# Kernel tuning notes

Measured on AMD Instinct MI355X. Metric: run time of the kernel, lower is better.

## Reference

```python
import jax, jax.numpy as jnp
import numpy as np
from jax import lax

K = 8          # neighbors
LOSS_NORM = 2  # Lp norm over coords


def setup_inputs() -> dict:
    key = jax.random.key(0)
    k1, k2, k3 = jax.random.split(key, 3)
    B, N = 4, 8192
    return {
        "pc_source": jax.random.normal(k1, (B, N, 3), dtype=jnp.float32),
        "pc_target": jax.random.normal(k2, (B, N, 3), dtype=jnp.float32),
        "pred_flow": jax.random.normal(k3, (B, N, 3), dtype=jnp.float32),
    }


def _knn_idx(query, points, k):
    # query: [B,N,3], points: [B,M,3] -> idx [B,N,k] of k nearest points per query
    # squared euclidean pairwise distances (ranking-equivalent to euclidean)
    q2 = jnp.sum(query * query, axis=-1, keepdims=True)          # [B,N,1]
    p2 = jnp.sum(points * points, axis=-1)[:, None, :]           # [B,1,M]
    d2 = q2 + p2 - 2.0 * jnp.einsum("bnd,bmd->bnm", query, points)  # [B,N,M]
    _, idx = lax.top_k(-d2, k)                                   # smallest-k
    return idx


def _gather_points(points, idx):
    # points: [B,M,3], idx: [B,N,k] -> [B,N,k,3]
    return jax.vmap(lambda p, i: p[i])(points, idx)


def reference(pc_source, pc_target, pred_flow):
    pc_pred = pc_source + pred_flow                               # [B,N,3]

    # knn indices are detached in the original (idx.detach())
    idx1 = _knn_idx(lax.stop_gradient(pc_pred), lax.stop_gradient(pc_target), K)
    nn1 = _gather_points(pc_target, idx1)                         # [B,N,K,3]
    diff1 = pc_pred[:, :, None, :] - nn1                          # [B,N,K,3]
    dist1 = jnp.linalg.norm(diff1, ord=LOSS_NORM, axis=-1).mean(axis=-1)  # [B,N]

    idx2 = _knn_idx(lax.stop_gradient(pc_target), lax.stop_gradient(pc_pred), K)
    nn2 = _gather_points(pc_pred, idx2)                           # [B,M,K,3]
    diff2 = pc_target[:, :, None, :] - nn2
    dist2 = jnp.linalg.norm(diff2, ord=LOSS_NORM, axis=-1).mean(axis=-1)  # [B,M]

    return (dist1 + dist2).mean()
```

## Files before the change

### kernel.cpp

```cpp
#include <hip/hip_runtime.h>
#include <math.h>

constexpr int B = 4;
constexpr int N = 8192;
constexpr int KNN = 8;
constexpr int NCELL = 4096;
constexpr int GSIZE = 16;
constexpr int NGRP = N / GSIZE;
constexpr int QPB = 64;
constexpr int WAVES = 8;
constexpr int NCB = 2 * B;

__device__ __forceinline__ void insert8(float (&d)[KNN], float tv) {
  float n0 = fminf(d[0], tv);
  float n1 = __builtin_amdgcn_fmed3f(d[0], d[1], tv);
  float n2 = __builtin_amdgcn_fmed3f(d[1], d[2], tv);
  float n3 = __builtin_amdgcn_fmed3f(d[2], d[3], tv);
  float n4 = __builtin_amdgcn_fmed3f(d[3], d[4], tv);
  float n5 = __builtin_amdgcn_fmed3f(d[4], d[5], tv);
  float n6 = __builtin_amdgcn_fmed3f(d[5], d[6], tv);
  float n7 = __builtin_amdgcn_fmed3f(d[6], d[7], tv);
  d[0] = n0; d[1] = n1; d[2] = n2; d[3] = n3;
  d[4] = n4; d[5] = n5; d[6] = n6; d[7] = n7;
}

__device__ __forceinline__ int morton3(int x, int y, int z) {
  int m = 0;
#pragma unroll
  for (int b = 0; b < 4; ++b)
    m |= (((x >> b) & 1) << (3 * b + 2)) | (((y >> b) & 1) << (3 * b + 1)) |
         (((z >> b) & 1) << (3 * b + 0));
  return m;
}

__device__ __forceinline__ int point_cell(float x, float y, float z) {
  int cx = (int)fminf(fmaxf((x + 4.0f) * 2.0f, 0.0f), 15.0f);
  int cy = (int)fminf(fmaxf((y + 4.0f) * 2.0f, 0.0f), 15.0f);
  int cz = (int)fminf(fmaxf((z + 4.0f) * 2.0f, 0.0f), 15.0f);
  return morton3(cx, cy, cz);
}

__global__ __launch_bounds__(1024) void prep_kernel(
    const float* __restrict__ src, const float* __restrict__ tgt,
    const float* __restrict__ flow, float4* __restrict__ pred_s,
    float4* __restrict__ tgt_s, float4* __restrict__ gbox,
    float* __restrict__ out) {
  __shared__ int hist[NCELL];
  __shared__ int wsum[16];
  __shared__ float4 pts[N];
  int tid = threadIdx.x, cb = blockIdx.x;
  int cloud = cb >> 2, batch = cb & 3;
  if (cb == 0 && tid == 0) out[0] = 0.0f;

  for (int i = tid; i < NCELL; i += 1024) hist[i] = 0;
  __syncthreads();

  const float* __restrict__ bp = (cloud == 0 ? src : tgt) + batch * N * 3;
  const float* __restrict__ bf = flow + batch * N * 3;
  float4 pt[8];
  int cell[8];
#pragma unroll
  for (int k = 0; k < 8; ++k) {
    int i = k * 1024 + tid;
    float x = bp[3 * i + 0], y = bp[3 * i + 1], z = bp[3 * i + 2];
    if (cloud == 0) { x += bf[3 * i + 0]; y += bf[3 * i + 1]; z += bf[3 * i + 2]; }
    pt[k] = make_float4(x, y, z, 0.5f * (x * x + y * y + z * z));
    cell[k] = point_cell(x, y, z);
    atomicAdd(&hist[cell[k]], 1);
  }
  __syncthreads();

  int b4 = tid * 4;
  int h0v = hist[b4 + 0], h1v = hist[b4 + 1];
  int h2v = hist[b4 + 2], h3v = hist[b4 + 3];
  int s = h0v + h1v + h2v + h3v;
  int lane = tid & 63, w = tid >> 6;
  int incl = s;
#pragma unroll
  for (int off = 1; off < 64; off <<= 1) {
    int u = __shfl_up(incl, off, 64);
    if (lane >= off) incl += u;
  }
  if (lane == 63) wsum[w] = incl;
  __syncthreads();
  if (tid < 16) {
    int v = wsum[tid], inc = v;
#pragma unroll
    for (int off = 1; off < 16; off <<= 1) {
      int u = __shfl_up(inc, off, 64);
      if (tid >= off) inc += u;
    }
    wsum[tid] = inc - v;
  }
  __syncthreads();
  int run = incl - s + wsum[w];
  hist[b4 + 0] = run; run += h0v;
  hist[b4 + 1] = run; run += h1v;
  hist[b4 + 2] = run; run += h2v;
  hist[b4 + 3] = run;
  __syncthreads();

#pragma unroll
  for (int k = 0; k < 8; ++k) {
    int pos = atomicAdd(&hist[cell[k]], 1);
    pts[pos] = pt[k];
  }
  __syncthreads();

  float4* __restrict__ dst = (cloud == 0 ? pred_s : tgt_s) + batch * N;
#pragma unroll
  for (int k = 0; k < 8; ++k) dst[k * 1024 + tid] = pts[k * 1024 + tid];

  if (tid < NGRP) {
    float lx = INFINITY, ly = INFINITY, lz = INFINITY;
    float hx = -INFINITY, hy = -INFINITY, hz = -INFINITY;
#pragma unroll
    for (int t = 0; t < GSIZE; ++t) {
      int j = (t + tid) & 15;
      float4 p = pts[tid * GSIZE + j];
      lx = fminf(lx, p.x); ly = fminf(ly, p.y); lz = fminf(lz, p.z);
      hx = fmaxf(hx, p.x); hy = fmaxf(hy, p.y); hz = fmaxf(hz, p.z);
    }
    gbox[cb * 2 * NGRP + 2 * tid + 0] = make_float4(lx, ly, lz, 0.0f);
    gbox[cb * 2 * NGRP + 2 * tid + 1] = make_float4(hx, hy, hz, 0.0f);
  }
}

__global__ __launch_bounds__(512, 8) void chamfer_kernel(
    const float4* __restrict__ pred_s, const float4* __restrict__ tgt_s,
    const float4* __restrict__ aabb, float* __restrict__ out) {
  int blk = blockIdx.x;
  int dir = blk >> 9;
  int batch = (blk >> 7) & 3;
  int chunk = blk & 127;
  const float4* __restrict__ qarr = (dir == 0 ? pred_s : tgt_s) + batch * N;
  const float4* __restrict__ parr = (dir == 0 ? tgt_s : pred_s) + batch * N;
  int ccb = (dir == 0 ? 4 + batch : batch);
  const float4* __restrict__ gb = aabb + ccb * (2 * NGRP);

  int lane = threadIdx.x & 63;
  int wv = __builtin_amdgcn_readfirstlane(threadIdx.x >> 6);

  __shared__ float4 boxes[2 * NGRP];
  __shared__ float part[WAVES][QPB][KNN + 1];

  for (int i = threadIdx.x; i < 2 * NGRP; i += 512) boxes[i] = gb[i];

  float4 q = qarr[chunk * QPB + lane];
  float nqx = -q.x, nqy = -q.y, nqz = -q.z;
  float two_qw = 2.0f * q.w;

  float d[KNN];
#pragma unroll
  for (int i = 0; i < KNN; ++i) d[i] = INFINITY;
  float thr = INFINITY;

  __syncthreads();

  int tc = (chunk * 4 + 6 - wv) >> 3;
  tc = max(0, min(63, tc));

  auto step = [&](int t) {
    int g = t * 8 + wv;
    float4 lo = boxes[2 * g + 0];
    float4 hi = boxes[2 * g + 1];
    float dx = fmaxf(fmaxf(lo.x - q.x, q.x - hi.x), 0.0f);
    float dy = fmaxf(fmaxf(lo.y - q.y, q.y - hi.y), 0.0f);
    float dz = fmaxf(fmaxf(lo.z - q.z, q.z - hi.z), 0.0f);
    float md = __builtin_fmaf(dx, dx, __builtin_fmaf(dy, dy, dz * dz));
    if (__ballot(md < thr)) {
      const float4* __restrict__ gp = parr + g * GSIZE;
#pragma unroll
      for (int j = 0; j < GSIZE; ++j) {
        float4 p = gp[j];
        float tv = __builtin_fmaf(nqx, p.x, __builtin_fmaf(nqy, p.y,
                   __builtin_fmaf(nqz, p.z, p.w)));
        insert8(d, tv);
      }
      float cand = __builtin_fmaf(2.0f, d[KNN - 1], two_qw) * 1.00001f + 1e-6f;
      thr = fminf(thr, cand);
    }
  };

  step(tc);
  if (tc + 1 < 64) step(tc + 1);

  part[wv][lane][0] = thr;
  __syncthreads();
  float tmin = part[0][lane][0];
#pragma unroll
  for (int s = 1; s < WAVES; ++s) tmin = fminf(tmin, part[s][lane][0]);
  thr = fminf(thr, tmin);
  __syncthreads();

  for (int t = tc + 2; t < 64; ++t) step(t);
  for (int t = tc - 1; t >= 0; --t) step(t);

#pragma unroll
  for (int i = 0; i < KNN; ++i) part[wv][lane][i] = d[i];
  __syncthreads();

  if (wv == 0) {
    float m[KNN];
#pragma unroll
    for (int i = 0; i < KNN; ++i) m[i] = part[0][lane][i];
    for (int s = 1; s < WAVES; ++s) {
#pragma unroll
      for (int i = 0; i < KNN; ++i) insert8(m, part[s][lane][i]);
    }
    float s_ = 0.0f;
#pragma unroll
    for (int i = 0; i < KNN; ++i) {
      float d2 = fmaxf(__builtin_fmaf(2.0f, m[i], two_qw), 0.0f);
      s_ += sqrtf(d2);
    }
    float val = s_ * (1.0f / KNN);
    for (int off = 32; off; off >>= 1) val += __shfl_down(val, off, 64);
    if (lane == 0) atomicAdd(out, val * (1.0f / (B * N)));
  }
}

extern "C" void kernel_launch(void* const* d_in, const int* in_sizes, int n_in,
                              void* d_out, int out_size, void* d_ws, size_t ws_size,
                              hipStream_t stream) {
  const float* src = (const float*)d_in[0];
  const float* tgt = (const float*)d_in[1];
  const float* flow = (const float*)d_in[2];
  float* out = (float*)d_out;

  float4* pred_s = (float4*)d_ws;
  float4* tgt_s = pred_s + B * N;
  float4* gbox = tgt_s + B * N;

  prep_kernel<<<NCB, 1024, 0, stream>>>(src, tgt, flow, pred_s, tgt_s, gbox,
                                        out);
  chamfer_kernel<<<2 * B * (N / QPB), 512, 0, stream>>>(pred_s, tgt_s, gbox, out);
}
```

Measured before the change: 126.2 us.

## Add window-level bounding boxes for hierarchical pruning and vectorize prep loads

After: 148.5 us. +17.6%, slower.

```diff
diff --git a/kernel.cpp b/kernel.cpp
--- a/kernel.cpp
+++ b/kernel.cpp
@@ -7,6 +7,7 @@
 constexpr int NCELL = 4096;
 constexpr int GSIZE = 16;
 constexpr int NGRP = N / GSIZE;
+constexpr int NWIN = 8;
 constexpr int QPB = 64;
 constexpr int WAVES = 8;
 constexpr int NCB = 2 * B;
@@ -44,10 +45,11 @@
     const float* __restrict__ src, const float* __restrict__ tgt,
     const float* __restrict__ flow, float4* __restrict__ pred_s,
     float4* __restrict__ tgt_s, float4* __restrict__ gbox,
-    float* __restrict__ out) {
+    float4* __restrict__ wbox, float* __restrict__ out) {
   __shared__ int hist[NCELL];
   __shared__ int wsum[16];
   __shared__ float4 pts[N];
+  __shared__ float4 wplo[16], wphi[16];
   int tid = threadIdx.x, cb = blockIdx.x;
   int cloud = cb >> 2, batch = cb & 3;
   if (cb == 0 && tid == 0) out[0] = 0.0f;
@@ -56,14 +58,28 @@
   __syncthreads();
 
   const float* __restrict__ bp = (cloud == 0 ? src : tgt) + batch * N * 3;
-  const float* __restrict__ bf = flow + batch * N * 3;
+  const float4* __restrict__ bp4 = reinterpret_cast<const float4*>(bp);
+  float4 s0 = bp4[6 * tid + 0], s1 = bp4[6 * tid + 1], s2 = bp4[6 * tid + 2];
+  float4 s3 = bp4[6 * tid + 3], s4 = bp4[6 * tid + 4], s5 = bp4[6 * tid + 5];
+  if (cloud == 0) {
+    const float4* __restrict__ bf4 =
+        reinterpret_cast<const float4*>(flow + batch * N * 3);
+    float4 f;
+    f = bf4[6 * tid + 0]; s0.x += f.x; s0.y += f.y; s0.z += f.z; s0.w += f.w;
+    f = bf4[6 * tid + 1]; s1.x += f.x; s1.y += f.y; s1.z += f.z; s1.w += f.w;
+    f = bf4[6 * tid + 2]; s2.x += f.x; s2.y += f.y; s2.z += f.z; s2.w += f.w;
+    f = bf4[6 * tid + 3]; s3.x += f.x; s3.y += f.y; s3.z += f.z; s3.w += f.w;
+    f = bf4[6 * tid + 4]; s4.x += f.x; s4.y += f.y; s4.z += f.z; s4.w += f.w;
+    f = bf4[6 * tid + 5]; s5.x += f.x; s5.y += f.y; s5.z += f.z; s5.w += f.w;
+  }
+  float px[8] = {s0.x, s0.w, s1.z, s2.y, s3.x, s3.w, s4.z, s5.y};
+  float py[8] = {s0.y, s1.x, s1.w, s2.z, s3.y, s4.x, s4.w, s5.z};
+  float pz[8] = {s0.z, s1.y, s2.x, s2.w, s3.z, s4.y, s5.x, s5.w};
   float4 pt[8];
   int cell[8];
 #pragma unroll
   for (int k = 0; k < 8; ++k) {
-    int i = k * 1024 + tid;
-    float x = bp[3 * i + 0], y = bp[3 * i + 1], z = bp[3 * i + 2];
-    if (cloud == 0) { x += bf[3 * i + 0]; y += bf[3 * i + 1]; z += bf[3 * i + 2]; }
+    float x = px[k], y = py[k], z = pz[k];
     pt[k] = make_float4(x, y, z, 0.5f * (x * x + y * y + z * z));
     cell[k] = point_cell(x, y, z);
     atomicAdd(&hist[cell[k]], 1);
@@ -111,6 +127,40 @@
 #pragma unroll
   for (int k = 0; k < 8; ++k) dst[k * 1024 + tid] = pts[k * 1024 + tid];
 
+  {
+    float lx = INFINITY, ly = INFINITY, lz = INFINITY;
+    float hx = -INFINITY, hy = -INFINITY, hz = -INFINITY;
+#pragma unroll
+    for (int t = 0; t < 8; ++t) {
+      int j = (t + tid) & 7;
+      float4 p = pts[tid * 8 + j];
+      lx = fminf(lx, p.x); ly = fminf(ly, p.y); lz = fminf(lz, p.z);
+      hx = fmaxf(hx, p.x); hy = fmaxf(hy, p.y); hz = fmaxf(hz, p.z);
+    }
+#pragma unroll
+    for (int m = 1; m < 64; m <<= 1) {
+      lx = fminf(lx, __shfl_xor(lx, m, 64));
+      ly = fminf(ly, __shfl_xor(ly, m, 64));
+      lz = fminf(lz, __shfl_xor(lz, m, 64));
+      hx = fmaxf(hx, __shfl_xor(hx, m, 64));
+      hy = fmaxf(hy, __shfl_xor(hy, m, 64));
+      hz = fmaxf(hz, __shfl_xor(hz, m, 64));
+    }
+    if (lane == 0) {
+      wplo[w] = make_float4(lx, ly, lz, 0.0f);
+      wphi[w] = make_float4(hx, hy, hz, 0.0f);
+    }
+  }
+  __syncthreads();
+  if (tid < NWIN) {
+    float4 a = wplo[2 * tid], b2 = wplo[2 * tid + 1];
+    float4 c = wphi[2 * tid], e = wphi[2 * tid + 1];
+    wbox[cb * 2 * NWIN + 2 * tid + 0] =
+        make_float4(fminf(a.x, b2.x), fminf(a.y, b2.y), fminf(a.z, b2.z), 0.0f);
+    wbox[cb * 2 * NWIN + 2 * tid + 1] =
+        make_float4(fmaxf(c.x, e.x), fmaxf(c.y, e.y), fmaxf(c.z, e.z), 0.0f);
+  }
+
   if (tid < NGRP) {
     float lx = INFINITY, ly = INFINITY, lz = INFINITY;
     float hx = -INFINITY, hy = -INFINITY, hz = -INFINITY;
@@ -128,7 +178,8 @@
 
 __global__ __launch_bounds__(512, 8) void chamfer_kernel(
     const float4* __restrict__ pred_s, const float4* __restrict__ tgt_s,
-    const float4* __restrict__ aabb, float* __restrict__ out) {
+    const float4* __restrict__ aabb, const float4* __restrict__ wb,
+    float* __restrict__ out) {
   int blk = blockIdx.x;
   int dir = blk >> 9;
   int batch = (blk >> 7) & 3;
@@ -137,14 +188,17 @@
   const float4* __restrict__ parr = (dir == 0 ? tgt_s : pred_s) + batch * N;
   int ccb = (dir == 0 ? 4 + batch : batch);
   const float4* __restrict__ gb = aabb + ccb * (2 * NGRP);
+  const float4* __restrict__ wbg = wb + ccb * (2 * NWIN);
 
   int lane = threadIdx.x & 63;
   int wv = __builtin_amdgcn_readfirstlane(threadIdx.x >> 6);
 
   __shared__ float4 boxes[2 * NGRP];
+  __shared__ float4 wbx[2 * NWIN];
   __shared__ float part[WAVES][QPB][KNN + 1];
 
   for (int i = threadIdx.x; i < 2 * NGRP; i += 512) boxes[i] = gb[i];
+  if (threadIdx.x < 2 * NWIN) wbx[threadIdx.x] = wbg[threadIdx.x];
 
   float4 q = qarr[chunk * QPB + lane];
   float nqx = -q.x, nqy = -q.y, nqz = -q.z;
@@ -159,15 +213,17 @@
 
   int tc = (chunk * 4 + 6 - wv) >> 3;
   tc = max(0, min(63, tc));
-
-  auto step = [&](int t) {
-    int g = t * 8 + wv;
-    float4 lo = boxes[2 * g + 0];
-    float4 hi = boxes[2 * g + 1];
+  int tc1 = (tc + 1 < 64) ? tc + 1 : -1;
+
+  auto boxmd = [&](float4 lo, float4 hi) {
     float dx = fmaxf(fmaxf(lo.x - q.x, q.x - hi.x), 0.0f);
     float dy = fmaxf(fmaxf(lo.y - q.y, q.y - hi.y), 0.0f);
     float dz = fmaxf(fmaxf(lo.z - q.z, q.z - hi.z), 0.0f);
-    float md = __builtin_fmaf(dx, dx, __builtin_fmaf(dy, dy, dz * dz));
+    return __builtin_fmaf(dx, dx, __builtin_fmaf(dy, dy, dz * dz));
+  };
+  auto step = [&](int t) {
+    int g = t * 8 + wv;
+    float md = boxmd(boxes[2 * g + 0], boxes[2 * g + 1]);
     if (__ballot(md < thr)) {
       const float4* __restrict__ gp = parr + g * GSIZE;
 #pragma unroll
@@ -175,7 +231,7 @@
         float4 p = gp[j];
         float tv = __builtin_fmaf(nqx, p.x, __builtin_fmaf(nqy, p.y,
                    __builtin_fmaf(nqz, p.z, p.w)));
-        insert8(d, tv);
+        if (__ballot(tv < d[KNN - 1])) insert8(d, tv);
       }
       float cand = __builtin_fmaf(2.0f, d[KNN - 1], two_qw) * 1.00001f + 1e-6f;
       thr = fminf(thr, cand);
@@ -183,7 +239,7 @@
   };
 
   step(tc);
-  if (tc + 1 < 64) step(tc + 1);
+  if (tc1 >= 0) step(tc1);
 
   part[wv][lane][0] = thr;
   __syncthreads();
@@ -193,8 +249,18 @@
   thr = fminf(thr, tmin);
   __syncthreads();
 
-  for (int t = tc + 2; t < 64; ++t) step(t);
-  for (int t = tc - 1; t >= 0; --t) step(t);
+  int wc = tc >> 3;
+  for (int k = 0; k < 15; ++k) {
+    int off = (k + 1) >> 1;
+    int o = (k & 1) ? wc + off : wc - off;
+    if (o < 0 || o > 7) continue;
+    float mdw = boxmd(wbx[2 * o + 0], wbx[2 * o + 1]);
+    if (!__ballot(mdw < thr)) continue;
+    for (int t = o * 8; t < o * 8 + 8; ++t) {
+      if (t == tc || t == tc1) continue;
+      step(t);
+    }
+  }
 
 #pragma unroll
   for (int i = 0; i < KNN; ++i) part[wv][lane][i] = d[i];
@@ -231,8 +297,10 @@
   float4* pred_s = (float4*)d_ws;
   float4* tgt_s = pred_s + B * N;
   float4* gbox = tgt_s + B * N;
+  float4* wbox = gbox + NCB * 2 * NGRP;
 
   prep_kernel<<<NCB, 1024, 0, stream>>>(src, tgt, flow, pred_s, tgt_s, gbox,
-                                        out);
-  chamfer_kernel<<<2 * B * (N / QPB), 512, 0, stream>>>(pred_s, tgt_s, gbox, out);
-}
+                                        wbox, out);
+  chamfer_kernel<<<2 * B * (N / QPB), 512, 0, stream>>>(pred_s, tgt_s, gbox,
+                                                        wbox, out);
+}
```
